# Performance work log

Measured on AMD Instinct MI355X. Metric: run time of the kernel, lower is better.

The kernel has to match this reference:

```python
import math
import jax, jax.numpy as jnp
import numpy as np

N_EXPERTS = 8
N_ACTIVE = 5
N_CAMP_A = 4
TEMPERATURE = math.e


def setup_inputs() -> dict:
    key = jax.random.key(0)
    ks = jax.random.split(key, 5)
    B, T, D, I = 4, 2048, 2048, 1024
    s = 0.02
    return {
        "x": jax.random.normal(ks[0], (B, T, D), jnp.float32),
        "Wr": jax.random.normal(ks[1], (D, N_EXPERTS), jnp.float32) * s,
        "Wg": jax.random.normal(ks[2], (N_EXPERTS, D, I), jnp.float32) * s,
        "Wu": jax.random.normal(ks[3], (N_EXPERTS, D, I), jnp.float32) * s,
        "Wd": jax.random.normal(ks[4], (N_EXPERTS, I, D), jnp.float32) * s,
    }


def _router_weights(x, Wr):
    # scores: (B,T,E)
    probs = jax.nn.softmax(jnp.einsum("btd,de->bte", x, Wr) / TEMPERATURE, axis=-1)
    _, topk_idx = jax.lax.top_k(probs, N_ACTIVE)          # (B,T,k)
    mask = jax.nn.one_hot(topk_idx, N_EXPERTS, dtype=probs.dtype).sum(axis=-2)
    w = probs * mask
    return w / (w.sum(axis=-1, keepdims=True) + 1e-8)


def reference(x, Wr, Wg, Wu, Wd):
    weights = _router_weights(x, Wr)                       # (B,T,E)
    # All experts run on full dense input (faithful to source loop), batched GEMMs.
    g = jnp.einsum("btd,edi->btei", x, Wg)                 # (B,T,E,I)
    u = jnp.einsum("btd,edi->btei", x, Wu)
    h = jax.nn.silu(g) * u
    eo = jnp.einsum("btei,eid->bted", h, Wd)               # (B,T,E,D)
    sign = jnp.concatenate([jnp.ones(N_CAMP_A), -jnp.ones(N_EXPERTS - N_CAMP_A)]).astype(x.dtype)
    output = jnp.einsum("bte,bted->btd", weights * sign, eo)  # out_a - out_g
    tension_scalar = jax.lax.stop_gradient(jnp.mean(output ** 2))
    return output, tension_scalar
```

## Files before the change

### kernel.cpp

```cpp
#include <hip/hip_runtime.h>
#include <cstdint>
#include <cstddef>


typedef short bf16x8 __attribute__((ext_vector_type(8)));
typedef float f32x4 __attribute__((ext_vector_type(4)));
typedef unsigned short u16;

typedef const unsigned int __attribute__((address_space(1)))* as1_u32p;
typedef unsigned int __attribute__((address_space(3)))* as3_u32p;

#define VMCNT6 asm volatile("s_waitcnt vmcnt(6)" ::: "memory")
#define VMCNT0 asm volatile("s_waitcnt vmcnt(0)" ::: "memory")
#define LGKM0  asm volatile("s_waitcnt lgkmcnt(0)" ::: "memory")
#define SBAR   __builtin_amdgcn_s_barrier()
#define SCHED0 __builtin_amdgcn_sched_barrier(0)
#define PRIO1  __builtin_amdgcn_s_setprio(1)
#define PRIO0  __builtin_amdgcn_s_setprio(0)
#define MFMA16(af, bf, cf) __builtin_amdgcn_mfma_f32_16x16x32_bf16(af, bf, cf, 0, 0, 0)

__device__ __forceinline__ u16 f2bf(float f) {
  unsigned u = __builtin_bit_cast(unsigned, f);
  u += 0x7fffu + ((u >> 16) & 1u);
  return (u16)(u >> 16);
}

__device__ __forceinline__ void gload16(const void* g, const u16* lds) {
  as1_u32p gp = (as1_u32p)(uintptr_t)g;
  as3_u32p lp = (as3_u32p)(unsigned)(uintptr_t)lds;
  __builtin_amdgcn_global_load_lds(gp, lp, 16, 0, 0);
}

__global__ __launch_bounds__(256) void router_kernel(
    const float* __restrict__ x, const float* __restrict__ Wr,
    float* __restrict__ Cw, u16* __restrict__ Xb) {
  const int l = threadIdx.x & 63;
  const int t = blockIdx.x * 4 + (threadIdx.x >> 6);
  const float* xr = x + (size_t)t * 2048;
  u16* xbr = Xb + (size_t)t * 2048;
  float p[8] = {0.f,0.f,0.f,0.f,0.f,0.f,0.f,0.f};
#pragma unroll
  for (int it = 0; it < 8; ++it) {
    const int d0 = it * 256 + l * 4;
    const float4 xv = *(const float4*)(xr + d0);
    unsigned lo = (unsigned)f2bf(xv.x) | ((unsigned)f2bf(xv.y) << 16);
    unsigned hi = (unsigned)f2bf(xv.z) | ((unsigned)f2bf(xv.w) << 16);
    *(unsigned*)(xbr + d0) = lo;
    *(unsigned*)(xbr + d0 + 2) = hi;
    const float xs[4] = {xv.x, xv.y, xv.z, xv.w};
#pragma unroll
    for (int jj = 0; jj < 4; ++jj) {
      const float4 w0 = *(const float4*)(Wr + (size_t)(d0 + jj) * 8);
      const float4 w1 = *(const float4*)(Wr + (size_t)(d0 + jj) * 8 + 4);
      p[0] += xs[jj] * w0.x; p[1] += xs[jj] * w0.y;
      p[2] += xs[jj] * w0.z; p[3] += xs[jj] * w0.w;
      p[4] += xs[jj] * w1.x; p[5] += xs[jj] * w1.y;
      p[6] += xs[jj] * w1.z; p[7] += xs[jj] * w1.w;
    }
  }
#pragma unroll
  for (int e = 0; e < 8; ++e) {
    float v = p[e];
#pragma unroll
    for (int off = 32; off > 0; off >>= 1) v += __shfl_xor(v, off, 64);
    p[e] = v;
  }
  constexpr float INV_TEMP = 0.36787944117144233f;
  float mx = -1e30f;
#pragma unroll
  for (int e = 0; e < 8; ++e) { p[e] *= INV_TEMP; mx = fmaxf(mx, p[e]); }
  float sum = 0.f;
#pragma unroll
  for (int e = 0; e < 8; ++e) { p[e] = __expf(p[e] - mx); sum += p[e]; }
  const float inv_sum = 1.f / sum;
#pragma unroll
  for (int e = 0; e < 8; ++e) p[e] *= inv_sum;
  unsigned sel = 0xFFu;
  for (int it = 0; it < 3; ++it) {
    float mn = 1e30f; int mi = 0;
#pragma unroll
    for (int e = 0; e < 8; ++e)
      if ((sel >> e) & 1u) { if (p[e] <= mn) { mn = p[e]; mi = e; } }
    sel &= ~(1u << mi);
  }
  float wsum = 0.f;
#pragma unroll
  for (int e = 0; e < 8; ++e) if ((sel >> e) & 1u) wsum += p[e];
  const float inv_w = 1.f / (wsum + 1e-8f);
  if (l == 0) {
#pragma unroll
    for (int e = 0; e < 8; ++e) {
      float v = ((sel >> e) & 1u) ? p[e] * inv_w : 0.f;
      Cw[(size_t)t * 8 + e] = (e < 4) ? v : -v;
    }
  }
}

__global__ __launch_bounds__(256) void build_idx(
    const float* __restrict__ Cw, int* __restrict__ idx, int* __restrict__ cnt) {
  const int e = blockIdx.x;
  const int tid = threadIdx.x;
  const int t0 = tid * 32;
  int c = 0;
#pragma unroll
  for (int j = 0; j < 32; ++j)
    if (Cw[(size_t)(t0 + j) * 8 + e] != 0.f) ++c;
  __shared__ int s[256];
  s[tid] = c;
  __syncthreads();
  for (int off = 1; off < 256; off <<= 1) {
    int v = (tid >= off) ? s[tid - off] : 0;
    __syncthreads();
    s[tid] += v;
    __syncthreads();
  }
  int o = e * 8192 + s[tid] - c;
  for (int j = 0; j < 32; ++j) {
    const int t = t0 + j;
    if (Cw[(size_t)t * 8 + e] != 0.f) idx[o++] = t;
  }
  if (tid == 255) cnt[e] = s[255];
}

__global__ __launch_bounds__(256) void tcvt_kernel(
    const float* __restrict__ in, u16* __restrict__ out,
    int R, int C, long long ZO, long long CS) {
  __shared__ float tile[32][33];
  const int z = blockIdx.z;
  const float* ib = in + (size_t)z * R * C;
  const int r0 = blockIdx.y * 32, c0 = blockIdx.x * 32;
  const int tx = threadIdx.x, ty = threadIdx.y;
#pragma unroll
  for (int j = 0; j < 4; ++j)
    tile[ty + j * 8][tx] = ib[(size_t)(r0 + ty + j * 8) * C + c0 + tx];
  __syncthreads();
#pragma unroll
  for (int j = 0; j < 4; ++j)
    out[(size_t)z * ZO + (size_t)(c0 + ty + j * 8) * CS + r0 + tx] =
        f2bf(tile[tx][ty + j * 8]);
}


__global__ __launch_bounds__(512, 2) void gemm1_8p(
    const u16* __restrict__ Xb, const u16* __restrict__ Wgt,
    const u16* __restrict__ Wut, const float* __restrict__ Cw,
    u16* __restrict__ Hp, const int* __restrict__ idx,
    const int* __restrict__ cnt, int p) {
  extern __shared__ u16 lds[];
  const int tid = threadIdx.x;
  const int l = tid & 63, w = tid >> 6;
  const int wr = w >> 2, wc = w & 3;
  const int lq = l >> 4, lr = l & 15;
  const int bid = blockIdx.x;
  const int work = (bid & 7) * 128 + (bid >> 3);
  const int mtile = work & 31;
  const int en = work >> 5;
  const int el = en >> 3, nt = en & 7;
  const int e = p * 4 + el;
  const int cnt_e = idx ? cnt[e] : 8192;
  const int base = mtile * 256;
  if (base >= cnt_e) return;
  const int* idxp = idx ? idx + (size_t)e * 8192 : nullptr;

  const u16* s0p = Wgt + (size_t)e * 2097152 + (size_t)nt * 128 * 2048;
  const u16* s1p = Wut + (size_t)e * 2097152 + (size_t)nt * 128 * 2048;

  const int lrow = tid >> 3;
  const int cgo = ((tid & 7) ^ (lrow & 7)) * 8;
  const int offB0 = lrow * 2048 + cgo;
  const int offB1 = offB0 + 64 * 2048;
  const int d0e = tid * 8, d1e = (512 + tid) * 8;

  auto gr = [&](int r) -> size_t {
    const int rr = r < cnt_e ? r : cnt_e - 1;
    return (size_t)(idxp ? idxp[rr] : rr) * 2048 + cgo;
  };
  const size_t a20 = gr(base + lrow);
  const size_t a21 = gr(base + 64 + lrow);
  const size_t a30 = gr(base + 128 + lrow);
  const size_t a31 = gr(base + 192 + lrow);

  const int NT = 32;
  auto stageB = [&](int tt, const u16* srcb, int u) {
    if (tt >= NT) return;
    u16* dst = lds + (tt & 1) * 32768 + u * 8192;
    const int kt = tt * 64;
    gload16(srcb + offB0 + kt, dst + d0e);
    gload16(srcb + offB1 + kt, dst + d1e);
  };
  auto stageA = [&](int tt, size_t b0, size_t b1, int u) {
    if (tt >= NT) return;
    u16* dst = lds + (tt & 1) * 32768 + u * 8192;
    const int kt = tt * 64;
    gload16(Xb + b0 + kt, dst + d0e);
    gload16(Xb + b1 + kt, dst + d1e);
  };

  const int xr = lr & 7;
  const int x0 = (lq ^ xr) * 8;
  const int x1 = ((4 + lq) ^ xr) * 8;
  const int aB = (2 + wr) * 8192 + lr * 64;
  const int gBo = (wc * 32 + lr) * 64;
  const int uBo = 8192 + (wc * 32 + lr) * 64;

  bf16x8 a[8][2], bg[2][2], bu[2][2];
  f32x4 ag[8][2], au[8][2];
#pragma unroll
  for (int mi = 0; mi < 8; ++mi)
#pragma unroll
    for (int ni = 0; ni < 2; ++ni) {
      ag[mi][ni] = (f32x4){0.f, 0.f, 0.f, 0.f};
      au[mi][ni] = (f32x4){0.f, 0.f, 0.f, 0.f};
    }

  stageB(0, s0p, 0); stageB(0, s1p, 1);
  stageA(0, a20, a21, 2); stageA(0, a30, a31, 3);
  stageB(1, s0p, 0); stageB(1, s1p, 1); stageA(1, a20, a21, 2);
  VMCNT6; SBAR;

  for (int t = 0; t < NT; ++t) {
    const u16* Lb = lds + (t & 1) * 32768;
    {
#pragma unroll
      for (int mi = 0; mi < 4; ++mi) {
        a[mi][0] = *(const bf16x8*)&Lb[aB + mi * 1024 + x0];
        a[mi][1] = *(const bf16x8*)&Lb[aB + mi * 1024 + x1];
      }
#pragma unroll
      for (int ni = 0; ni < 2; ++ni) {
        bg[ni][0] = *(const bf16x8*)&Lb[gBo + ni * 1024 + x0];
        bg[ni][1] = *(const bf16x8*)&Lb[gBo + ni * 1024 + x1];
      }
      stageA(t + 1, a30, a31, 3);
      SBAR; LGKM0; SCHED0;
      PRIO1;
#pragma unroll
      for (int mi = 0; mi < 4; ++mi)
#pragma unroll
        for (int ni = 0; ni < 2; ++ni)
#pragma unroll
          for (int kk = 0; kk < 2; ++kk)
            ag[mi][ni] = MFMA16(a[mi][kk], bg[ni][kk], ag[mi][ni]);
      PRIO0; SCHED0; SBAR;
    }
    {
#pragma unroll
      for (int ni = 0; ni < 2; ++ni) {
        bu[ni][0] = *(const bf16x8*)&Lb[uBo + ni * 1024 + x0];
        bu[ni][1] = *(const bf16x8*)&Lb[uBo + ni * 1024 + x1];
      }
      stageB(t + 2, s0p, 0);
      SBAR; LGKM0; SCHED0;
      PRIO1;
#pragma unroll
      for (int mi = 0; mi < 4; ++mi)
#pragma unroll
        for (int ni = 0; ni < 2; ++ni)
#pragma unroll
          for (int kk = 0; kk < 2; ++kk)
            au[mi][ni] = MFMA16(a[mi][kk], bu[ni][kk], au[mi][ni]);
      PRIO0; SCHED0; SBAR;
    }
    {
#pragma unroll
      for (int mi = 4; mi < 8; ++mi) {
        a[mi][0] = *(const bf16x8*)&Lb[aB + mi * 1024 + x0];
        a[mi][1] = *(const bf16x8*)&Lb[aB + mi * 1024 + x1];
      }
      stageB(t + 2, s1p, 1);
      SBAR; LGKM0; SCHED0;
      PRIO1;
#pragma unroll
      for (int mi = 4; mi < 8; ++mi)
#pragma unroll
        for (int ni = 0; ni < 2; ++ni)
#pragma unroll
          for (int kk = 0; kk < 2; ++kk)
            ag[mi][ni] = MFMA16(a[mi][kk], bg[ni][kk], ag[mi][ni]);
      PRIO0; SCHED0; SBAR;
    }
    {
      stageA(t + 2, a20, a21, 2);
      if (t < NT - 2) { VMCNT6; } else if (t == NT - 2) { VMCNT0; }
      SBAR; LGKM0; SCHED0;
      PRIO1;
#pragma unroll
      for (int mi = 4; mi < 8; ++mi)
#pragma unroll
        for (int ni = 0; ni < 2; ++ni)
#pragma unroll
          for (int kk = 0; kk < 2; ++kk)
            au[mi][ni] = MFMA16(a[mi][kk], bu[ni][kk], au[mi][ni]);
      PRIO0; SCHED0; SBAR;
    }
  }

#pragma unroll
  for (int mi = 0; mi < 8; ++mi) {
#pragma unroll
    for (int j = 0; j < 4; ++j) {
      const int rl = wr * 128 + mi * 16 + lq * 4 + j;
      const int grow = base + rl;
      if (grow < cnt_e) {
        const int orow = idxp ? idxp[grow] : grow;
        const float c = Cw[(size_t)orow * 8 + e];
#pragma unroll
        for (int ni = 0; ni < 2; ++ni) {
          const float g = ag[mi][ni][j], u = au[mi][ni][j];
          const float h = g * (1.f / (1.f + __expf(-g))) * u * c;
          Hp[(size_t)orow * 4096 + el * 1024 + nt * 128 + wc * 32 + ni * 16 + lr] =
              f2bf(h);
        }
      }
    }
  }
}

__global__ __launch_bounds__(512, 2) void gemm2_8p(
    const u16* __restrict__ Hp, const u16* __restrict__ Wdt,
    float* __restrict__ out, int koff, int accum) {
  extern __shared__ u16 lds[];
  const int tid = threadIdx.x;
  const int l = tid & 63, w = tid >> 6;
  const int wr = w >> 2, wc = w & 3;
  const int lq = l >> 4, lr = l & 15;
  const int bid = blockIdx.x;
  const int work = (bid & 7) * 32 + (bid >> 3);
  const int mtile = work & 31, ntile = work >> 5;
  const u16* gA = Hp + (size_t)mtile * 256 * 4096;
  const u16* gB = Wdt + (size_t)ntile * 256 * 8192 + koff;
  const u16* s0p = gB;
  const u16* s1p = gB + (size_t)128 * 8192;
  const u16* s2p = gA;
  const u16* s3p = gA + (size_t)128 * 4096;
  const int NT = 64;

  const int row0 = tid >> 3,          cg0 = (tid & 7) ^ (row0 & 7);
  const int row1 = (512 + tid) >> 3,  cg1 = ((512 + tid) & 7) ^ (row1 & 7);
  const int offA0 = row0 * 4096 + cg0 * 8, offA1 = row1 * 4096 + cg1 * 8;
  const int offB0 = row0 * 8192 + cg0 * 8, offB1 = row1 * 8192 + cg1 * 8;
  const int d0e = tid * 8, d1e = (512 + tid) * 8;

  auto stageA = [&](int tt, const u16* srcb, int u) {
    if (tt >= NT) return;
    u16* dst = lds + (tt & 1) * 32768 + u * 8192;
    const int kt = tt * 64;
    gload16(srcb + (size_t)(offA0 + kt), dst + d0e);
    gload16(srcb + (size_t)(offA1 + kt), dst + d1e);
  };
  auto stageB = [&](int tt, const u16* srcb, int u) {
    if (tt >= NT) return;
    u16* dst = lds + (tt & 1) * 32768 + u * 8192;
    const int kt = tt * 64;
    gload16(srcb + (size_t)(offB0 + kt), dst + d0e);
    gload16(srcb + (size_t)(offB1 + kt), dst + d1e);
  };

  const int xr = lr & 7;
  const int x0 = (lq ^ xr) * 8;
  const int x1 = ((4 + lq) ^ xr) * 8;
  const int aB = (2 + wr) * 8192 + lr * 64;
  const int bB = (wc >> 1) * 8192 + ((wc & 1) * 64 + lr) * 64;

  bf16x8 a[8][2], b[4][2];
  f32x4 acc[8][4];
#pragma unroll
  for (int mi = 0; mi < 8; ++mi)
#pragma unroll
    for (int ni = 0; ni < 4; ++ni) acc[mi][ni] = (f32x4){0.f, 0.f, 0.f, 0.f};

  stageB(0, s0p, 0); stageB(0, s1p, 1); stageA(0, s2p, 2); stageA(0, s3p, 3);
  stageB(1, s0p, 0); stageB(1, s1p, 1); stageA(1, s2p, 2);
  VMCNT6; SBAR;

  for (int t = 0; t < NT; ++t) {
    const u16* Lb = lds + (t & 1) * 32768;
    {
#pragma unroll
      for (int mi = 0; mi < 4; ++mi) {
        a[mi][0] = *(const bf16x8*)&Lb[aB + mi * 1024 + x0];
        a[mi][1] = *(const bf16x8*)&Lb[aB + mi * 1024 + x1];
      }
#pragma unroll
      for (int ni = 0; ni < 2; ++ni) {
        b[ni][0] = *(const bf16x8*)&Lb[bB + ni * 1024 + x0];
        b[ni][1] = *(const bf16x8*)&Lb[bB + ni * 1024 + x1];
      }
      if (wc < 2) {
#pragma unroll
        for (int ni = 2; ni < 4; ++ni) {
          b[ni][0] = *(const bf16x8*)&Lb[bB + ni * 1024 + x0];
          b[ni][1] = *(const bf16x8*)&Lb[bB + ni * 1024 + x1];
        }
      }
      stageA(t + 1, s3p, 3);
      SBAR; LGKM0; SCHED0;
      PRIO1;
#pragma unroll
      for (int mi = 0; mi < 4; ++mi)
#pragma unroll
        for (int ni = 0; ni < 2; ++ni)
#pragma unroll
          for (int kk = 0; kk < 2; ++kk)
            acc[mi][ni] = MFMA16(a[mi][kk], b[ni][kk], acc[mi][ni]);
      PRIO0; SCHED0; SBAR;
    }
    {
      if (wc >= 2) {
#pragma unroll
        for (int ni = 2; ni < 4; ++ni) {
          b[ni][0] = *(const bf16x8*)&Lb[bB + ni * 1024 + x0];
          b[ni][1] = *(const bf16x8*)&Lb[bB + ni * 1024 + x1];
        }
      }
      stageB(t + 2, s0p, 0);
      SBAR; LGKM0; SCHED0;
      PRIO1;
#pragma unroll
      for (int mi = 0; mi < 4; ++mi)
#pragma unroll
        for (int ni = 2; ni < 4; ++ni)
#pragma unroll
          for (int kk = 0; kk < 2; ++kk)
            acc[mi][ni] = MFMA16(a[mi][kk], b[ni][kk], acc[mi][ni]);
      PRIO0; SCHED0; SBAR;
    }
    {
#pragma unroll
      for (int mi = 4; mi < 8; ++mi) {
        a[mi][0] = *(const bf16x8*)&Lb[aB + mi * 1024 + x0];
        a[mi][1] = *(const bf16x8*)&Lb[aB + mi * 1024 + x1];
      }
      stageB(t + 2, s1p, 1);
      SBAR; LGKM0; SCHED0;
      PRIO1;
#pragma unroll
      for (int mi = 4; mi < 8; ++mi)
#pragma unroll
        for (int ni = 2; ni < 4; ++ni)
#pragma unroll
          for (int kk = 0; kk < 2; ++kk)
            acc[mi][ni] = MFMA16(a[mi][kk], b[ni][kk], acc[mi][ni]);
      PRIO0; SCHED0; SBAR;
    }
    {
      stageA(t + 2, s2p, 2);
      if (t < NT - 2) { VMCNT6; } else if (t == NT - 2) { VMCNT0; }
      SBAR; LGKM0; SCHED0;
      PRIO1;
#pragma unroll
      for (int mi = 4; mi < 8; ++mi)
#pragma unroll
        for (int ni = 0; ni < 2; ++ni)
#pragma unroll
          for (int kk = 0; kk < 2; ++kk)
            acc[mi][ni] = MFMA16(a[mi][kk], b[ni][kk], acc[mi][ni]);
      PRIO0; SCHED0; SBAR;
    }
  }

#pragma unroll
  for (int mi = 0; mi < 8; ++mi)
#pragma unroll
    for (int ni = 0; ni < 4; ++ni)
#pragma unroll
      for (int j = 0; j < 4; ++j) {
        const int row = mtile * 256 + wr * 128 + mi * 16 + lq * 4 + j;
        const int col = ntile * 256 + wc * 64 + ni * 16 + lr;
        const size_t idx2 = (size_t)row * 2048 + col;
        float v = acc[mi][ni][j];
        if (accum) v += out[idx2];
        out[idx2] = v;
      }
}

__global__ __launch_bounds__(256) void sqsum_partial(
    const float* __restrict__ out, float* __restrict__ part, int n4) {
  float s = 0.f;
  const int idx = blockIdx.x * 256 + threadIdx.x;
  const int stride = gridDim.x * 256;
  for (int i = idx; i < n4; i += stride) {
    const float4 v = ((const float4*)out)[i];
    s += v.x * v.x + v.y * v.y + v.z * v.z + v.w * v.w;
  }
#pragma unroll
  for (int off = 32; off > 0; off >>= 1) s += __shfl_down(s, off, 64);
  __shared__ float ls[4];
  if ((threadIdx.x & 63) == 0) ls[threadIdx.x >> 6] = s;
  __syncthreads();
  if (threadIdx.x == 0) part[blockIdx.x] = ls[0] + ls[1] + ls[2] + ls[3];
}

__global__ __launch_bounds__(256) void sqsum_final(
    const float* __restrict__ part, float* __restrict__ dst, int np, float scale) {
  float s = 0.f;
  for (int i = threadIdx.x; i < np; i += 256) s += part[i];
#pragma unroll
  for (int off = 32; off > 0; off >>= 1) s += __shfl_down(s, off, 64);
  __shared__ float ls[4];
  if ((threadIdx.x & 63) == 0) ls[threadIdx.x >> 6] = s;
  __syncthreads();
  if (threadIdx.x == 0) dst[0] = (ls[0] + ls[1] + ls[2] + ls[3]) * scale;
}

extern "C" void kernel_launch(void* const* d_in, const int* in_sizes, int n_in,
                              void* d_out, int out_size, void* d_ws, size_t ws_size,
                              hipStream_t stream) {
  (void)in_sizes; (void)n_in; (void)out_size;
  const float* x  = (const float*)d_in[0];
  const float* Wr = (const float*)d_in[1];
  const float* Wg = (const float*)d_in[2];
  const float* Wu = (const float*)d_in[3];
  const float* Wd = (const float*)d_in[4];
  float* out = (float*)d_out;
  char* ws = (char*)d_ws;
  u16*   Xb   = (u16*)(ws);
  u16*   Wgt  = (u16*)(ws + 33554432);
  u16*   Wut  = (u16*)(ws + 67108864);
  u16*   Wdt  = (u16*)(ws + 100663296);
  u16*   Hp   = (u16*)(ws + 134217728);
  float* Cw   = (float*)(ws + 201326592);
  float* part = (float*)(ws + 201588736);
  const bool SPARSE = ws_size >= 201855008u;
  int* idxbuf = SPARSE ? (int*)(ws + 201592832) : nullptr;
  int* cntbuf = SPARSE ? (int*)(ws + 201854976) : nullptr;

  (void)hipFuncSetAttribute((const void*)gemm1_8p,
                            hipFuncAttributeMaxDynamicSharedMemorySize, 131072);
  (void)hipFuncSetAttribute((const void*)gemm2_8p,
                            hipFuncAttributeMaxDynamicSharedMemorySize, 131072);

  router_kernel<<<2048, 256, 0, stream>>>(x, Wr, Cw, Xb);
  if (SPARSE) build_idx<<<8, 256, 0, stream>>>(Cw, idxbuf, cntbuf);

  dim3 tb(32, 8);
  tcvt_kernel<<<dim3(32, 64, 8), tb, 0, stream>>>(Wg, Wgt, 2048, 1024, 2097152LL, 2048LL);
  tcvt_kernel<<<dim3(32, 64, 8), tb, 0, stream>>>(Wu, Wut, 2048, 1024, 2097152LL, 2048LL);
  tcvt_kernel<<<dim3(64, 32, 8), tb, 0, stream>>>(Wd, Wdt, 1024, 2048, 1024LL, 8192LL);

  for (int p = 0; p < 2; ++p) {
    if (SPARSE) (void)hipMemsetAsync(Hp, 0, 67108864, stream);
    gemm1_8p<<<1024, 512, 131072, stream>>>(Xb, Wgt, Wut, Cw, Hp,
                                            idxbuf, cntbuf, p);
    gemm2_8p<<<256, 512, 131072, stream>>>(Hp, Wdt, out, p * 4096, p);
  }

  sqsum_partial<<<1024, 256, 0, stream>>>(out, part, 16777216 / 4);
  sqsum_final<<<1, 256, 0, stream>>>(part, out + 16777216, 1024, 1.f / 16777216.f);
}
```

Baseline: 822.0 us.

## Fuse squared-sum into GEMM2 epilogue, selective Hp zeroing, larger transpose tiles

The squared-sum reduction moves into the second-pass GEMM2 epilogue, which writes per-block partials, so the separate full read of the output is dropped. The full memset of the hidden buffer is replaced by a kernel that zeroes only the rows of experts a token does not use. The weight transpose-convert kernel now uses 64x64 tiles, and an early partial lgkmcnt wait is added before barriers in both GEMMs. Together these aim to cut memory traffic and launch overhead, at the cost of more LDS per transpose block and a slightly longer GEMM2 epilogue.

```diff
diff --git a/kernel.cpp b/kernel.cpp
--- a/kernel.cpp
+++ b/kernel.cpp
@@ -13,6 +13,7 @@
 #define VMCNT6 asm volatile("s_waitcnt vmcnt(6)" ::: "memory")
 #define VMCNT0 asm volatile("s_waitcnt vmcnt(0)" ::: "memory")
 #define LGKM0  asm volatile("s_waitcnt lgkmcnt(0)" ::: "memory")
+#define LGKM8  asm volatile("s_waitcnt lgkmcnt(8)" ::: "memory")
 #define SBAR   __builtin_amdgcn_s_barrier()
 #define SCHED0 __builtin_amdgcn_sched_barrier(0)
 #define PRIO1  __builtin_amdgcn_s_setprio(1)
@@ -122,22 +123,37 @@
   if (tid == 255) cnt[e] = s[255];
 }
 
+__global__ __launch_bounds__(256) void zerofill(
+    const float* __restrict__ Cw, u16* __restrict__ Hp, int p) {
+  const int t = blockIdx.x * 4 + (threadIdx.x >> 6);
+  const int l = threadIdx.x & 63;
+  bf16x8* rowp = (bf16x8*)(Hp + (size_t)t * 4096);
+  const bf16x8 z = {0, 0, 0, 0, 0, 0, 0, 0};
+#pragma unroll
+  for (int el = 0; el < 4; ++el) {
+    if (Cw[(size_t)t * 8 + p * 4 + el] == 0.f) {
+      rowp[el * 128 + l] = z;
+      rowp[el * 128 + 64 + l] = z;
+    }
+  }
+}
+
 __global__ __launch_bounds__(256) void tcvt_kernel(
     const float* __restrict__ in, u16* __restrict__ out,
     int R, int C, long long ZO, long long CS) {
-  __shared__ float tile[32][33];
+  __shared__ float tile[64][65];
   const int z = blockIdx.z;
   const float* ib = in + (size_t)z * R * C;
-  const int r0 = blockIdx.y * 32, c0 = blockIdx.x * 32;
+  const int r0 = blockIdx.y * 64, c0 = blockIdx.x * 64;
   const int tx = threadIdx.x, ty = threadIdx.y;
 #pragma unroll
-  for (int j = 0; j < 4; ++j)
-    tile[ty + j * 8][tx] = ib[(size_t)(r0 + ty + j * 8) * C + c0 + tx];
+  for (int j = 0; j < 16; ++j)
+    tile[ty + j * 4][tx] = ib[(size_t)(r0 + ty + j * 4) * C + c0 + tx];
   __syncthreads();
 #pragma unroll
-  for (int j = 0; j < 4; ++j)
-    out[(size_t)z * ZO + (size_t)(c0 + ty + j * 8) * CS + r0 + tx] =
-        f2bf(tile[tx][ty + j * 8]);
+  for (int j = 0; j < 16; ++j)
+    out[(size_t)z * ZO + (size_t)(c0 + ty + j * 4) * CS + r0 + tx] =
+        f2bf(tile[tx][ty + j * 4]);
 }
 
 
@@ -232,7 +248,7 @@
         bg[ni][1] = *(const bf16x8*)&Lb[gBo + ni * 1024 + x1];
       }
       stageA(t + 1, a30, a31, 3);
-      SBAR; LGKM0; SCHED0;
+      LGKM8; SBAR; LGKM0; SCHED0;
       PRIO1;
 #pragma unroll
       for (int mi = 0; mi < 4; ++mi)
@@ -318,7 +334,7 @@
 
 __global__ __launch_bounds__(512, 2) void gemm2_8p(
     const u16* __restrict__ Hp, const u16* __restrict__ Wdt,
-    float* __restrict__ out, int koff, int accum) {
+    float* __restrict__ out, float* __restrict__ part, int koff, int accum) {
   extern __shared__ u16 lds[];
   const int tid = threadIdx.x;
   const int l = tid & 63, w = tid >> 6;
@@ -394,7 +410,7 @@
         }
       }
       stageA(t + 1, s3p, 3);
-      SBAR; LGKM0; SCHED0;
+      LGKM8; SBAR; LGKM0; SCHED0;
       PRIO1;
 #pragma unroll
       for (int mi = 0; mi < 4; ++mi)
@@ -459,6 +475,7 @@
     }
   }
 
+  float sq = 0.f;
 #pragma unroll
   for (int mi = 0; mi < 8; ++mi)
 #pragma unroll
@@ -469,26 +486,23 @@
         const int col = ntile * 256 + wc * 64 + ni * 16 + lr;
         const size_t idx2 = (size_t)row * 2048 + col;
         float v = acc[mi][ni][j];
-        if (accum) v += out[idx2];
+        if (accum) { v += out[idx2]; sq += v * v; }
         out[idx2] = v;
       }
-}
-
-__global__ __launch_bounds__(256) void sqsum_partial(
-    const float* __restrict__ out, float* __restrict__ part, int n4) {
-  float s = 0.f;
-  const int idx = blockIdx.x * 256 + threadIdx.x;
-  const int stride = gridDim.x * 256;
-  for (int i = idx; i < n4; i += stride) {
-    const float4 v = ((const float4*)out)[i];
-    s += v.x * v.x + v.y * v.y + v.z * v.z + v.w * v.w;
-  }
-#pragma unroll
-  for (int off = 32; off > 0; off >>= 1) s += __shfl_down(s, off, 64);
-  __shared__ float ls[4];
-  if ((threadIdx.x & 63) == 0) ls[threadIdx.x >> 6] = s;
-  __syncthreads();
-  if (threadIdx.x == 0) part[blockIdx.x] = ls[0] + ls[1] + ls[2] + ls[3];
+  if (accum) {
+#pragma unroll
+    for (int off = 32; off > 0; off >>= 1) sq += __shfl_down(sq, off, 64);
+    __syncthreads();
+    float* sm = (float*)lds;
+    if (l == 0) sm[w] = sq;
+    __syncthreads();
+    if (tid == 0) {
+      float tot = 0.f;
+#pragma unroll
+      for (int i = 0; i < 8; ++i) tot += sm[i];
+      part[bid] = tot;
+    }
+  }
 }
 
 __global__ __launch_bounds__(256) void sqsum_final(
@@ -533,18 +547,17 @@
   router_kernel<<<2048, 256, 0, stream>>>(x, Wr, Cw, Xb);
   if (SPARSE) build_idx<<<8, 256, 0, stream>>>(Cw, idxbuf, cntbuf);
 
-  dim3 tb(32, 8);
-  tcvt_kernel<<<dim3(32, 64, 8), tb, 0, stream>>>(Wg, Wgt, 2048, 1024, 2097152LL, 2048LL);
-  tcvt_kernel<<<dim3(32, 64, 8), tb, 0, stream>>>(Wu, Wut, 2048, 1024, 2097152LL, 2048LL);
-  tcvt_kernel<<<dim3(64, 32, 8), tb, 0, stream>>>(Wd, Wdt, 1024, 2048, 1024LL, 8192LL);
+  dim3 tb(64, 4);
+  tcvt_kernel<<<dim3(16, 32, 8), tb, 0, stream>>>(Wg, Wgt, 2048, 1024, 2097152LL, 2048LL);
+  tcvt_kernel<<<dim3(16, 32, 8), tb, 0, stream>>>(Wu, Wut, 2048, 1024, 2097152LL, 2048LL);
+  tcvt_kernel<<<dim3(32, 16, 8), tb, 0, stream>>>(Wd, Wdt, 1024, 2048, 1024LL, 8192LL);
 
   for (int p = 0; p < 2; ++p) {
-    if (SPARSE) (void)hipMemsetAsync(Hp, 0, 67108864, stream);
+    if (SPARSE) zerofill<<<2048, 256, 0, stream>>>(Cw, Hp, p);
     gemm1_8p<<<1024, 512, 131072, stream>>>(Xb, Wgt, Wut, Cw, Hp,
                                             idxbuf, cntbuf, p);
-    gemm2_8p<<<256, 512, 131072, stream>>>(Hp, Wdt, out, p * 4096, p);
-  }
-
-  sqsum_partial<<<1024, 256, 0, stream>>>(out, part, 16777216 / 4);
-  sqsum_final<<<1, 256, 0, stream>>>(part, out + 16777216, 1024, 1.f / 16777216.f);
-}
+    gemm2_8p<<<256, 512, 131072, stream>>>(Hp, Wdt, out, part, p * 4096, p);
+  }
+
+  sqsum_final<<<1, 256, 0, stream>>>(part, out + 16777216, 256, 1.f / 16777216.f);
+}
```

Result: no change. 806.4 us (-1.9%).
